# Optimization experiments

Measured on AMD Instinct MI355X. Metric: run time of the kernel, lower is better.

Reference implementation:

```python
import jax, jax.numpy as jnp
import numpy as np

KERNEL_EPS = 1e-4  # performer-pytorch softmax_kernel eps


def _softmax_kernel(data, projection, is_query):
    # data: [b, h, n, d]; projection: [m, d]
    d = data.shape[-1]
    m = projection.shape[0]
    data_normalizer = d ** -0.25
    ratio = m ** -0.5
    # random-feature logits: [b, h, n, m]
    data_dash = jnp.einsum('bhnd,md->bhnm', data * data_normalizer, projection)
    # ||x||^2 / 2 * normalizer^2, [b, h, n, 1]
    diag = 0.5 * (data_normalizer ** 2) * jnp.sum(data * data, axis=-1, keepdims=True)
    if is_query:
        stab = jnp.max(data_dash, axis=-1, keepdims=True)
    else:
        stab = jnp.max(data_dash)  # global max, as in performer-pytorch
    return ratio * (jnp.exp(data_dash - diag - stab) + KERNEL_EPS)


def _linear_attention(q, k, v):
    # q, k: [b, h, n, m] random features; v: [b, h, n, e]
    k_cumsum = jnp.sum(k, axis=-2)                                   # [b, h, m]
    d_inv = 1.0 / jnp.einsum('bhnm,bhm->bhn', q, k_cumsum)           # [b, h, n]
    context = jnp.einsum('bhnm,bhne->bhme', k, v)                    # [b, h, m, e]
    return jnp.einsum('bhme,bhnm,bhn->bhne', context, q, d_inv)      # [b, h, n, e]


def setup_inputs() -> dict:
    key = jax.random.key(0)
    kq, kk, kv = jax.random.split(key, 3)
    b, h, n, d = 8, 16, 4096, 64
    nb_features = 256
    query = jax.random.normal(kq, (b, h, n, d), dtype=jnp.float32)
    key_t = jax.random.normal(kk, (b, h, n, d), dtype=jnp.float32)
    value = jax.random.normal(kv, (b, h, n, d), dtype=jnp.float32)
    # Gaussian orthogonal random matrix (performer-pytorch, scaling=0):
    # stack of d x d orthonormal blocks, rows rescaled to chi(d) norms.
    rng = np.random.RandomState(0)
    blocks = []
    for _ in range(nb_features // d + 1):
        qmat, _ = np.linalg.qr(rng.randn(d, d))
        blocks.append(qmat.T)
    proj = np.concatenate(blocks, axis=0)[:nb_features]
    multiplier = np.linalg.norm(rng.randn(nb_features, d), axis=1)
    projection = jnp.asarray(multiplier[:, None] * proj, dtype=jnp.float32)
    return {"query": query, "key": key_t, "value": value, "projection": projection}


def reference(query, key, value, projection):
    q_prime = _softmax_kernel(query, projection, is_query=True)   # [b,h,n,m]
    k_prime = _softmax_kernel(key, projection, is_query=False)    # [b,h,n,m]
    return _linear_attention(q_prime, k_prime, value)             # [b,h,n,e]
```

## Files before the change

### kernel.cpp

```cpp
#include <hip/hip_runtime.h>
#include <hip/hip_bf16.h>

typedef __attribute__((ext_vector_type(4))) float f32x4;
typedef __attribute__((ext_vector_type(8))) short short8;
typedef __attribute__((ext_vector_type(4))) unsigned short us4;
typedef __attribute__((ext_vector_type(4))) unsigned int u32x4;

#define BH_ 128
#define N_ 4096
#define LOG2E 1.4426950408889634f
#define NORML (0.35355339059327373f * LOG2E)
#define DIAGL (0.0625f * LOG2E)
#define EPSF 1e-4f

#if __has_builtin(__builtin_amdgcn_exp2f)
#define EXP2F(x) __builtin_amdgcn_exp2f(x)
#else
#define EXP2F(x) exp2f(x)
#endif

#define BARRIER_LGKM() asm volatile("s_waitcnt lgkmcnt(0)\ns_barrier" ::: "memory")

static __device__ __forceinline__ unsigned short f2bf(float f) {
  return __bfloat16_as_ushort(__float2bfloat16(f));
}
static __device__ __forceinline__ float bf2f(unsigned short s) {
  return __uint_as_float(((unsigned int)s) << 16);
}
static __device__ __forceinline__ us4 cvt4(f32x4 x) {
  us4 r;
  r[0] = f2bf(x[0]); r[1] = f2bf(x[1]); r[2] = f2bf(x[2]); r[3] = f2bf(x[3]);
  return r;
}
static __device__ __forceinline__ unsigned int pk2bf(float lo, float hi) {
  unsigned int r;
  asm("v_cvt_pk_bf16_f32 %0, %1, %2" : "=v"(r) : "v"(lo), "v"(hi));
  return r;
}

static __device__ __forceinline__ int posm(int m) {
  return (m & 0xE0) | ((m & 0xC) << 1) | ((m & 0x10) >> 2) | (m & 3);
}

__global__ void perf_prep(const float* __restrict__ proj,
                          unsigned short* __restrict__ projb) {
  int i = blockIdx.x * 256 + threadIdx.x;
  projb[i] = f2bf(proj[i] * NORML);
}

__global__ __launch_bounds__(256, 2)
void perf_kpass(const float* __restrict__ kp, const float* __restrict__ vp,
                const float* __restrict__ proj, float* __restrict__ ctxp,
                float* __restrict__ kexpp, float* __restrict__ vsump,
                unsigned int* __restrict__ gmaxb, int nchunk) {
  const int bh = blockIdx.x & (BH_ - 1);
  const int chunk = blockIdx.x >> 7;
  const int chunkrows = N_ / nchunk;
  const int tiles = chunkrows >> 5;
  const int t = threadIdx.x;
  const int wid = t >> 6;
  const int lane = t & 63;
  const int g = lane >> 4;
  const int c = lane & 15;

  __shared__ __align__(16) unsigned short sX[32][72];
  __shared__ __align__(16) unsigned short sVt[64][40];
  __shared__ __align__(16) unsigned short sW[256][40];
  __shared__ float sDiag[32];
  __shared__ float sVsum[64];
  __shared__ float sGm[4];

  short8 pfrag[4][2];
#pragma unroll
  for (int mt = 0; mt < 4; ++mt)
#pragma unroll
    for (int kk = 0; kk < 2; ++kk) {
      const float* src = proj + (wid * 64 + mt * 16 + c) * 64 + kk * 32 + g * 8;
      short8 v;
#pragma unroll
      for (int j = 0; j < 8; ++j) v[j] = (short)f2bf(src[j] * NORML);
      pfrag[mt][kk] = v;
    }

  f32x4 ctx[4][4];
#pragma unroll
  for (int i = 0; i < 4; ++i)
#pragma unroll
    for (int j = 0; j < 4; ++j) ctx[i][j] = (f32x4){0.f, 0.f, 0.f, 0.f};

  float kexpreg[4] = {0.f, 0.f, 0.f, 0.f};
  float vsum0 = 0.f, vsum1 = 0.f, vsum2 = 0.f, vsum3 = 0.f;
  float gm = -1e30f;

  const float* kb0 = kp + ((size_t)bh * N_ + (size_t)chunk * chunkrows) * 64;
  const float* vb0 = vp + ((size_t)bh * N_ + (size_t)chunk * chunkrows) * 64;

  f32x4 kx[2], vx[2];
#pragma unroll
  for (int hh = 0; hh < 2; ++hh) {
    int f = t + hh * 256;
    kx[hh] = *(const f32x4*)(kb0 + (f >> 4) * 64 + (f & 15) * 4);
    vx[hh] = *(const f32x4*)(vb0 + (f >> 4) * 64 + (f & 15) * 4);
  }

  for (int nt = 0; nt < tiles; ++nt) {
    BARRIER_LGKM();
#pragma unroll
    for (int hh = 0; hh < 2; ++hh) {
      int f = t + hh * 256;
      int row = f >> 4;
      int c4 = f & 15;
      f32x4 x = kx[hh];
      float ss = x[0] * x[0] + x[1] * x[1] + x[2] * x[2] + x[3] * x[3];
      ss += __shfl_xor(ss, 1);
      ss += __shfl_xor(ss, 2);
      ss += __shfl_xor(ss, 4);
      ss += __shfl_xor(ss, 8);
      if (c4 == 0) sDiag[row] = DIAGL * ss;
      *(us4*)&sX[row][c4 * 4] = cvt4(x);
      f32x4 vv = vx[hh];
      vsum0 += vv[0]; vsum1 += vv[1]; vsum2 += vv[2]; vsum3 += vv[3];
#pragma unroll
      for (int jj = 0; jj < 4; ++jj) {
        int j = (jj + t) & 3;
        float val = (j == 0) ? vv[0] : (j == 1) ? vv[1] : (j == 2) ? vv[2] : vv[3];
        sVt[c4 * 4 + j][row] = f2bf(val);
      }
    }
    if (nt + 1 < tiles) {
      const float* kb = kb0 + (nt + 1) * 2048;
      const float* vb = vb0 + (nt + 1) * 2048;
#pragma unroll
      for (int hh = 0; hh < 2; ++hh) {
        int f = t + hh * 256;
        kx[hh] = *(const f32x4*)(kb + (f >> 4) * 64 + (f & 15) * 4);
        vx[hh] = *(const f32x4*)(vb + (f >> 4) * 64 + (f & 15) * 4);
      }
    }
    BARRIER_LGKM();

    short8 afr[2][2];
#pragma unroll
    for (int nh1 = 0; nh1 < 2; ++nh1)
#pragma unroll
      for (int kk = 0; kk < 2; ++kk)
        afr[nh1][kk] = *(const short8*)&sX[nh1 * 16 + c][kk * 32 + g * 8];

    f32x4 acc1[2][4];
#pragma unroll
    for (int i = 0; i < 2; ++i)
#pragma unroll
      for (int j = 0; j < 4; ++j) acc1[i][j] = (f32x4){0.f, 0.f, 0.f, 0.f};
#pragma unroll
    for (int kk = 0; kk < 2; ++kk)
#pragma unroll
      for (int nh1 = 0; nh1 < 2; ++nh1)
#pragma unroll
        for (int mt = 0; mt < 4; ++mt)
          acc1[nh1][mt] = __builtin_amdgcn_mfma_f32_16x16x32_bf16(
              afr[nh1][kk], pfrag[mt][kk], acc1[nh1][mt], 0, 0, 0);

#pragma unroll
    for (int nh1 = 0; nh1 < 2; ++nh1)
#pragma unroll
      for (int mt = 0; mt < 4; ++mt) {
        int m = wid * 64 + mt * 16 + c;
        unsigned short wp[4];
#pragma unroll
        for (int r = 0; r < 4; ++r) {
          float dd = acc1[nh1][mt][r];
          gm = fmaxf(gm, dd);
          int n = nh1 * 16 + g * 4 + r;
          float w = EXP2F(dd - sDiag[n]);
          unsigned short wb = f2bf(w);
          kexpreg[mt] += bf2f(wb);
          wp[r] = wb;
        }
        us4 w4 = {wp[0], wp[1], wp[2], wp[3]};
        *(us4*)&sW[m][nh1 * 16 + g * 4] = w4;
      }

    short8 awt[4], bvv[4];
#pragma unroll
    for (int mt2 = 0; mt2 < 4; ++mt2)
      awt[mt2] = *(const short8*)&sW[wid * 64 + mt2 * 16 + c][g * 8];
#pragma unroll
    for (int et = 0; et < 4; ++et)
      bvv[et] = *(const short8*)&sVt[et * 16 + c][g * 8];
#pragma unroll
    for (int mt2 = 0; mt2 < 4; ++mt2)
#pragma unroll
      for (int et = 0; et < 4; ++et)
        ctx[mt2][et] = __builtin_amdgcn_mfma_f32_16x16x32_bf16(
            awt[mt2], bvv[et], ctx[mt2][et], 0, 0, 0);
  }

#pragma unroll
  for (int mt2 = 0; mt2 < 4; ++mt2)
#pragma unroll
    for (int et = 0; et < 4; ++et) {
      int m0 = wid * 64 + mt2 * 16 + g * 4;
      int e = et * 16 + c;
      size_t base = (((size_t)chunk * BH_ + bh) * 64 + e) * 256 + m0;
      *(f32x4*)(ctxp + base) = ctx[mt2][et];
    }
#pragma unroll
  for (int mt = 0; mt < 4; ++mt) {
    float s = kexpreg[mt];
    s += __shfl_xor(s, 16);
    s += __shfl_xor(s, 32);
    if (lane < 16)
      kexpp[((size_t)chunk * BH_ + bh) * 256 + wid * 64 + mt * 16 + lane] = s;
  }
  if (t < 64) sVsum[t] = 0.f;
  __syncthreads();
  atomicAdd(&sVsum[(t & 15) * 4 + 0], vsum0);
  atomicAdd(&sVsum[(t & 15) * 4 + 1], vsum1);
  atomicAdd(&sVsum[(t & 15) * 4 + 2], vsum2);
  atomicAdd(&sVsum[(t & 15) * 4 + 3], vsum3);
  __syncthreads();
  if (t < 64) vsump[((size_t)chunk * BH_ + bh) * 64 + t] = sVsum[t];

  gm = fmaxf(gm, __shfl_xor(gm, 1));
  gm = fmaxf(gm, __shfl_xor(gm, 2));
  gm = fmaxf(gm, __shfl_xor(gm, 4));
  gm = fmaxf(gm, __shfl_xor(gm, 8));
  gm = fmaxf(gm, __shfl_xor(gm, 16));
  gm = fmaxf(gm, __shfl_xor(gm, 32));
  if (lane == 0) sGm[wid] = gm;
  __syncthreads();
  if (t == 0) {
    float mm = fmaxf(fmaxf(sGm[0], sGm[1]), fmaxf(sGm[2], sGm[3]));
    atomicMax((int*)gmaxb, __float_as_int(mm));
  }
}

__global__ void perf_rescale(const float* __restrict__ ctxp,
                             const float* __restrict__ kexpp,
                             const float* __restrict__ vsump,
                             unsigned short* __restrict__ ctxt,
                             unsigned short* __restrict__ kchi,
                             unsigned short* __restrict__ kclo,
                             const unsigned int* __restrict__ gmaxb, int nchunk) {
  const int bh = blockIdx.x >> 3;
  const int es = blockIdx.x & 7;
  const int t = threadIdx.x;
  const int pos = posm(t);
  const float gmax = __uint_as_float(*gmaxb);
  const float s = EXP2F(-gmax);
  if (es == 0) {
    float acc = 0.f;
    for (int cc = 0; cc < nchunk; ++cc)
      acc += kexpp[((size_t)cc * BH_ + bh) * 256 + t];
    float kcv = s * acc + EPSF * (float)N_;
    unsigned short hi = f2bf(kcv);
    kchi[bh * 256 + pos] = hi;
    kclo[bh * 256 + pos] = f2bf(kcv - bf2f(hi));
  }
  for (int e = es * 8; e < es * 8 + 8; ++e) {
    float vs = 0.f;
    for (int cc = 0; cc < nchunk; ++cc)
      vs += vsump[((size_t)cc * BH_ + bh) * 64 + e];
    float a2 = 0.f;
    for (int cc = 0; cc < nchunk; ++cc)
      a2 += ctxp[(((size_t)cc * BH_ + bh) * 64 + e) * 256 + t];
    ctxt[((size_t)bh * 64 + e) * 256 + pos] = f2bf(s * a2 + EPSF * vs);
  }
}

__global__ __launch_bounds__(256, 2)
void perf_qpass(const float* __restrict__ qp,
                const unsigned short* __restrict__ projb,
                const unsigned short* __restrict__ ctxt,
                const unsigned short* __restrict__ kchi,
                const unsigned short* __restrict__ kclo,
                float* __restrict__ outp) {
  const int bh = blockIdx.x >> 3;
  const int chunk = blockIdx.x & 7;
  const int t = threadIdx.x;
  const int wid = t >> 6;
  const int lane = t & 63;
  const int g = lane >> 4;
  const int c = lane & 15;

  __shared__ __align__(16) unsigned short sP[256 * 64];
  __shared__ __align__(16) unsigned short sC[64 * 256];
  __shared__ __align__(16) unsigned short sC2[16 * 256];

  const unsigned short* csrc = ctxt + (size_t)bh * 64 * 256;
  const unsigned short* khib = kchi + bh * 256;
  const unsigned short* klob = kclo + bh * 256;

  const float* qbase = qp + ((size_t)bh * N_ + chunk * 512 + wid * 128) * 64;
  float* obase = outp + ((size_t)bh * N_ + chunk * 512 + wid * 128) * 64;

  const float* q0 = qbase + (size_t)c * 64 + g * 8;
  f32x4 xp0 = *(const f32x4*)(q0);
  f32x4 xp1 = *(const f32x4*)(q0 + 4);
  f32x4 xp2 = *(const f32x4*)(q0 + 32);
  f32x4 xp3 = *(const f32x4*)(q0 + 36);

#pragma unroll
  for (int rep = 0; rep < 8; ++rep) {
    int e = rep * 2048 + t * 8;
    {
      int row = e >> 6, slot = (e & 63) >> 3;
      short8 v = *(const short8*)(projb + e);
      *(short8*)((char*)sP + row * 128 + ((slot ^ (row & 7)) << 4)) = v;
    }
    {
      int row = e >> 8, slot = (e & 255) >> 3;
      short8 v = *(const short8*)(csrc + e);
      *(short8*)((char*)sC + row * 512 + ((slot ^ (row & 7)) << 4)) = v;
    }
  }
#pragma unroll
  for (int rep = 0; rep < 2; ++rep) {
    int e = rep * 2048 + t * 8;
    int row = e >> 8, col = e & 255, slot = col >> 3;
    short8 v = {0, 0, 0, 0, 0, 0, 0, 0};
    if (row == 0) v = *(const short8*)(khib + col);
    if (row == 1) v = *(const short8*)(klob + col);
    *(short8*)((char*)sC2 + row * 512 + ((slot ^ (row & 7)) << 4)) = v;
  }
  __syncthreads();

  const int gsw = (g ^ (c & 3)) << 4;
  const int b6 = (c >> 2) & 1;
  const int pb0 = c * 128 + (b6 << 6) + gsw;
  const int pb1 = c * 128 + ((1 ^ b6) << 6) + gsw;
  const char* spc = (const char*)sP;
  const char* scc = (const char*)sC + c * 512;
  const char* sc2c = (const char*)sC2 + c * 512;

#pragma unroll 1
  for (int tt = 0; tt < 8; ++tt) {
    f32x4 x0 = xp0, x1 = xp1, x2 = xp2, x3 = xp3;
    if (tt + 1 < 8) {
      const float* qn = qbase + ((size_t)((tt + 1) * 16 + c)) * 64 + g * 8;
      xp0 = *(const f32x4*)(qn);
      xp1 = *(const f32x4*)(qn + 4);
      xp2 = *(const f32x4*)(qn + 32);
      xp3 = *(const f32x4*)(qn + 36);
    }
    float ss = x0[0]*x0[0] + x0[1]*x0[1] + x0[2]*x0[2] + x0[3]*x0[3]
             + x1[0]*x1[0] + x1[1]*x1[1] + x1[2]*x1[2] + x1[3]*x1[3]
             + x2[0]*x2[0] + x2[1]*x2[1] + x2[2]*x2[2] + x2[3]*x2[3]
             + x3[0]*x3[0] + x3[1]*x3[1] + x3[2]*x3[2] + x3[3]*x3[3];
    ss += __shfl_xor(ss, 16);
    ss += __shfl_xor(ss, 32);
    const float diag = DIAGL * ss;

    short8 xb0, xb1;
#pragma unroll
    for (int j = 0; j < 4; ++j) {
      xb0[j] = (short)f2bf(x0[j]);
      xb0[j + 4] = (short)f2bf(x1[j]);
      xb1[j] = (short)f2bf(x2[j]);
      xb1[j + 4] = (short)f2bf(x3[j]);
    }

    f32x4 acc1[16];
#pragma unroll
    for (int mt = 0; mt < 16; ++mt) acc1[mt] = (f32x4){0.f, 0.f, 0.f, 0.f};
    short8 Ak0[4], Ak1[4], Bk0[4], Bk1[4];
#pragma unroll
    for (int i = 0; i < 4; ++i) {
      Ak0[i] = *(const short8*)(spc + i * 2048 + pb0);
      Ak1[i] = *(const short8*)(spc + i * 2048 + pb1);
    }
#pragma unroll
    for (int i = 0; i < 4; ++i) {
      Bk0[i] = *(const short8*)(spc + (4 + i) * 2048 + pb0);
      Bk1[i] = *(const short8*)(spc + (4 + i) * 2048 + pb1);
    }
#pragma unroll
    for (int i = 0; i < 4; ++i) {
      acc1[i] = __builtin_amdgcn_mfma_f32_16x16x32_bf16(Ak0[i], xb0, acc1[i], 0, 0, 0);
      acc1[i] = __builtin_amdgcn_mfma_f32_16x16x32_bf16(Ak1[i], xb1, acc1[i], 0, 0, 0);
    }
#pragma unroll
    for (int i = 0; i < 4; ++i) {
      Ak0[i] = *(const short8*)(spc + (8 + i) * 2048 + pb0);
      Ak1[i] = *(const short8*)(spc + (8 + i) * 2048 + pb1);
    }
#pragma unroll
    for (int i = 0; i < 4; ++i) {
      acc1[4 + i] = __builtin_amdgcn_mfma_f32_16x16x32_bf16(Bk0[i], xb0, acc1[4 + i], 0, 0, 0);
      acc1[4 + i] = __builtin_amdgcn_mfma_f32_16x16x32_bf16(Bk1[i], xb1, acc1[4 + i], 0, 0, 0);
    }
#pragma unroll
    for (int i = 0; i < 4; ++i) {
      Bk0[i] = *(const short8*)(spc + (12 + i) * 2048 + pb0);
      Bk1[i] = *(const short8*)(spc + (12 + i) * 2048 + pb1);
    }
#pragma unroll
    for (int i = 0; i < 4; ++i) {
      acc1[8 + i] = __builtin_amdgcn_mfma_f32_16x16x32_bf16(Ak0[i], xb0, acc1[8 + i], 0, 0, 0);
      acc1[8 + i] = __builtin_amdgcn_mfma_f32_16x16x32_bf16(Ak1[i], xb1, acc1[8 + i], 0, 0, 0);
    }
#pragma unroll
    for (int i = 0; i < 4; ++i) {
      acc1[12 + i] = __builtin_amdgcn_mfma_f32_16x16x32_bf16(Bk0[i], xb0, acc1[12 + i], 0, 0, 0);
      acc1[12 + i] = __builtin_amdgcn_mfma_f32_16x16x32_bf16(Bk1[i], xb1, acc1[12 + i], 0, 0, 0);
    }

    float mx = acc1[0][0];
#pragma unroll
    for (int mt = 0; mt < 16; ++mt)
#pragma unroll
      for (int r = 0; r < 4; ++r) mx = fmaxf(mx, acc1[mt][r]);
    mx = fmaxf(mx, __shfl_xor(mx, 16));
    mx = fmaxf(mx, __shfl_xor(mx, 32));
    const float base = diag + mx;

    uint2 qtp[16];
#pragma unroll
    for (int mt = 0; mt < 16; ++mt) {
      float qa = EXP2F(acc1[mt][0] - base) + EPSF;
      float qb = EXP2F(acc1[mt][1] - base) + EPSF;
      float qc = EXP2F(acc1[mt][2] - base) + EPSF;
      float qd = EXP2F(acc1[mt][3] - base) + EPSF;
      qtp[mt].x = pk2bf(qa, qb);
      qtp[mt].y = pk2bf(qc, qd);
    }

    f32x4 acc2[5];
#pragma unroll
    for (int et = 0; et < 5; ++et) acc2[et] = (f32x4){0.f, 0.f, 0.f, 0.f};
#pragma unroll
    for (int w = 0; w < 8; ++w) {
      const int colb = ((w ^ b6) << 6) + gsw;
      short8 b0 = *(const short8*)(scc + colb);
      short8 b1 = *(const short8*)(scc + colb + 8192);
      short8 b2 = *(const short8*)(scc + colb + 16384);
      short8 b3 = *(const short8*)(scc + colb + 24576);
      short8 bd = *(const short8*)(sc2c + colb);
      u32x4 av = {qtp[2 * w].x, qtp[2 * w].y, qtp[2 * w + 1].x, qtp[2 * w + 1].y};
      short8 a = __builtin_bit_cast(short8, av);
      acc2[0] = __builtin_amdgcn_mfma_f32_16x16x32_bf16(a, b0, acc2[0], 0, 0, 0);
      acc2[1] = __builtin_amdgcn_mfma_f32_16x16x32_bf16(a, b1, acc2[1], 0, 0, 0);
      acc2[2] = __builtin_amdgcn_mfma_f32_16x16x32_bf16(a, b2, acc2[2], 0, 0, 0);
      acc2[3] = __builtin_amdgcn_mfma_f32_16x16x32_bf16(a, b3, acc2[3], 0, 0, 0);
      acc2[4] = __builtin_amdgcn_mfma_f32_16x16x32_bf16(a, bd, acc2[4], 0, 0, 0);
    }

    float* ot = obase + (size_t)tt * 16 * 64;
#pragma unroll
    for (int r = 0; r < 4; ++r) {
      float den = __shfl(acc2[4][r], g * 16) + __shfl(acc2[4][r], g * 16 + 1);
      float rinv = 1.0f / den;
      int n = g * 4 + r;
#pragma unroll
      for (int et = 0; et < 4; ++et)
        ot[(size_t)n * 64 + et * 16 + c] = acc2[et][r] * rinv;
    }
  }
}

extern "C" void kernel_launch(void* const* d_in, const int* in_sizes, int n_in,
                              void* d_out, int out_size, void* d_ws, size_t ws_size,
                              hipStream_t stream) {
  (void)in_sizes; (void)n_in; (void)out_size;
  const float* qp = (const float*)d_in[0];
  const float* kp = (const float*)d_in[1];
  const float* vp = (const float*)d_in[2];
  const float* proj = (const float*)d_in[3];
  float* outp = (float*)d_out;

  int nchunk = 8;
  while (nchunk > 1) {
    size_t fl = 64 + (size_t)nchunk * (2097152 + 32768 + 8192);
    size_t needed = fl * 4 + (size_t)(2097152 + 32768 + 32768 + 16384) * 2;
    if (needed <= ws_size) break;
    nchunk >>= 1;
  }

  float* wsf = (float*)d_ws;
  unsigned int* gmaxb = (unsigned int*)d_ws;
  float* ctxp = wsf + 64;
  float* kexpp = ctxp + (size_t)nchunk * 128 * 64 * 256;
  float* vsump = kexpp + (size_t)nchunk * 128 * 256;
  unsigned short* ctxt = (unsigned short*)(vsump + (size_t)nchunk * 128 * 64);
  unsigned short* kchi = ctxt + (size_t)128 * 64 * 256;
  unsigned short* kclo = kchi + 128 * 256;
  unsigned short* projb = kclo + 128 * 256;

  hipMemsetAsync(d_ws, 0, 16, stream);
  hipLaunchKernelGGL(perf_prep, dim3(64), dim3(256), 0, stream, proj, projb);
  hipLaunchKernelGGL(perf_kpass, dim3(128 * nchunk), dim3(256), 0, stream,
                     kp, vp, proj, ctxp, kexpp, vsump, gmaxb, nchunk);
  hipLaunchKernelGGL(perf_rescale, dim3(128 * 8), dim3(256), 0, stream,
                     ctxp, kexpp, vsump, ctxt, kchi, kclo, gmaxb, nchunk);
  hipLaunchKernelGGL(perf_qpass, dim3(128 * 8), dim3(256), 0, stream,
                     qp, projb, ctxt, kchi, kclo, outp);
}
```

Baseline: 198.7 us.

## Keep exp weights in registers as MFMA operand and double-buffer LDS tiles

The exponentiated feature weights are now packed straight from the first MFMA's accumulator layout into the A-operand fragment of the second MFMA, so the sW shared-memory round trip is gone. To keep the K dimension consistent, the V-transpose store uses a permuted row index. The sX, sVt and sDiag buffers are double-buffered by tile parity, which removes the barrier at the top of the loop. The aim is to cut LDS traffic and synchronisation, at the cost of a nontrivial index permutation that has to line up exactly with the MFMA register layout.

```diff
diff --git a/kernel.cpp b/kernel.cpp
--- a/kernel.cpp
+++ b/kernel.cpp
@@ -63,10 +63,9 @@
   const int g = lane >> 4;
   const int c = lane & 15;
 
-  __shared__ __align__(16) unsigned short sX[32][72];
-  __shared__ __align__(16) unsigned short sVt[64][40];
-  __shared__ __align__(16) unsigned short sW[256][40];
-  __shared__ float sDiag[32];
+  __shared__ __align__(16) unsigned short sX[2][32][72];
+  __shared__ __align__(16) unsigned short sVt[2][64][40];
+  __shared__ float sDiag[2][32];
   __shared__ float sVsum[64];
   __shared__ float sGm[4];
 
@@ -104,7 +103,7 @@
   }
 
   for (int nt = 0; nt < tiles; ++nt) {
-    BARRIER_LGKM();
+    const int buf = nt & 1;
 #pragma unroll
     for (int hh = 0; hh < 2; ++hh) {
       int f = t + hh * 256;
@@ -116,15 +115,16 @@
       ss += __shfl_xor(ss, 2);
       ss += __shfl_xor(ss, 4);
       ss += __shfl_xor(ss, 8);
-      if (c4 == 0) sDiag[row] = DIAGL * ss;
-      *(us4*)&sX[row][c4 * 4] = cvt4(x);
+      if (c4 == 0) sDiag[buf][row] = DIAGL * ss;
+      *(us4*)&sX[buf][row][c4 * 4] = cvt4(x);
       f32x4 vv = vx[hh];
       vsum0 += vv[0]; vsum1 += vv[1]; vsum2 += vv[2]; vsum3 += vv[3];
+      const int ks = ((row >> 2) & 3) * 8 + (row >> 4) * 4 + (row & 3);
 #pragma unroll
       for (int jj = 0; jj < 4; ++jj) {
         int j = (jj + t) & 3;
         float val = (j == 0) ? vv[0] : (j == 1) ? vv[1] : (j == 2) ? vv[2] : vv[3];
-        sVt[c4 * 4 + j][row] = f2bf(val);
+        sVt[buf][c4 * 4 + j][ks] = f2bf(val);
       }
     }
     if (nt + 1 < tiles) {
@@ -144,7 +144,7 @@
     for (int nh1 = 0; nh1 < 2; ++nh1)
 #pragma unroll
       for (int kk = 0; kk < 2; ++kk)
-        afr[nh1][kk] = *(const short8*)&sX[nh1 * 16 + c][kk * 32 + g * 8];
+        afr[nh1][kk] = *(const short8*)&sX[buf][nh1 * 16 + c][kk * 32 + g * 8];
 
     f32x4 acc1[2][4];
 #pragma unroll
@@ -160,39 +160,33 @@
           acc1[nh1][mt] = __builtin_amdgcn_mfma_f32_16x16x32_bf16(
               afr[nh1][kk], pfrag[mt][kk], acc1[nh1][mt], 0, 0, 0);
 
-#pragma unroll
-    for (int nh1 = 0; nh1 < 2; ++nh1)
-#pragma unroll
-      for (int mt = 0; mt < 4; ++mt) {
-        int m = wid * 64 + mt * 16 + c;
-        unsigned short wp[4];
+    short8 wfrag[4];
+#pragma unroll
+    for (int mt = 0; mt < 4; ++mt) {
+#pragma unroll
+      for (int nh1 = 0; nh1 < 2; ++nh1)
 #pragma unroll
         for (int r = 0; r < 4; ++r) {
           float dd = acc1[nh1][mt][r];
           gm = fmaxf(gm, dd);
           int n = nh1 * 16 + g * 4 + r;
-          float w = EXP2F(dd - sDiag[n]);
+          float w = EXP2F(dd - sDiag[buf][n]);
           unsigned short wb = f2bf(w);
           kexpreg[mt] += bf2f(wb);
-          wp[r] = wb;
+          wfrag[mt][nh1 * 4 + r] = (short)wb;
         }
-        us4 w4 = {wp[0], wp[1], wp[2], wp[3]};
-        *(us4*)&sW[m][nh1 * 16 + g * 4] = w4;
-      }
-
-    short8 awt[4], bvv[4];
-#pragma unroll
-    for (int mt2 = 0; mt2 < 4; ++mt2)
-      awt[mt2] = *(const short8*)&sW[wid * 64 + mt2 * 16 + c][g * 8];
+    }
+
+    short8 bvv[4];
 #pragma unroll
     for (int et = 0; et < 4; ++et)
-      bvv[et] = *(const short8*)&sVt[et * 16 + c][g * 8];
+      bvv[et] = *(const short8*)&sVt[buf][et * 16 + c][g * 8];
 #pragma unroll
     for (int mt2 = 0; mt2 < 4; ++mt2)
 #pragma unroll
       for (int et = 0; et < 4; ++et)
         ctx[mt2][et] = __builtin_amdgcn_mfma_f32_16x16x32_bf16(
-            awt[mt2], bvv[et], ctx[mt2][et], 0, 0, 0);
+            wfrag[mt2], bvv[et], ctx[mt2][et], 0, 0, 0);
   }
 
 #pragma unroll
```

Measured after the change: 201.0 us. Within noise of the previous version (+1.2%).
